# Kernel optimization log

Hardware: AMD Instinct MI355X
Metric: run time of the kernel (lower is better)

## Reference

```python
import jax, jax.numpy as jnp
import numpy as np

DIM = 1024
HEADS = 16
DIM_HEAD = 64
INNER = HEADS * DIM_HEAD  # 1024
EPS = 1e-5


def layer_norm(x, g, b):
    mu = jnp.mean(x, axis=-1, keepdims=True)
    var = jnp.var(x, axis=-1, keepdims=True)
    return (x - mu) * jax.lax.rsqrt(var + EPS) * g + b


def setup_inputs() -> dict:
    key = jax.random.key(0)
    ks = jax.random.split(key, 8)
    s = 0.02
    return {
        "x": jax.random.normal(ks[0], (2, 2048, DIM), dtype=jnp.float32),
        "w_qkv": jax.random.normal(ks[1], (DIM, 3 * INNER), dtype=jnp.float32) * s,
        "w_out": jax.random.normal(ks[2], (INNER, DIM), dtype=jnp.float32) * s,
        "b_out": jnp.zeros((DIM,), jnp.float32),
        "g1": jnp.ones((DIM,), jnp.float32),
        "bt1": jnp.zeros((DIM,), jnp.float32),
        "g2": jnp.ones((DIM,), jnp.float32),
        "bt2": jnp.zeros((DIM,), jnp.float32),
        "w1": jax.random.normal(ks[3], (DIM, DIM), dtype=jnp.float32) * s,  # ff hidden = dim_out = DIM
        "b1": jnp.zeros((DIM,), jnp.float32),
        "w2": jax.random.normal(ks[4], (DIM, DIM), dtype=jnp.float32) * s,
        "b2": jnp.zeros((DIM,), jnp.float32),
    }


def reference(x, w_qkv, w_out, b_out, g1, bt1, g2, bt2, w1, b1, w2, b2):
    b, n, _ = x.shape
    scale = DIM_HEAD ** (-0.5)
    x_in = x
    xl = layer_norm(x, g1, bt1)
    qkv = xl @ w_qkv  # [b, n, 3*inner]
    q, k, v = jnp.split(qkv, 3, axis=-1)
    def split_heads(t):
        return t.reshape(b, n, HEADS, DIM_HEAD).transpose(0, 2, 1, 3)  # b h n d
    q, k, v = map(split_heads, (q, k, v))
    dots = jnp.einsum('bhid,bhjd->bhij', q, k) * scale
    attn = jax.nn.softmax(dots, axis=-1)
    out = jnp.einsum('bhij,bhjd->bhid', attn, v)
    out = out.transpose(0, 2, 1, 3).reshape(b, n, INNER)
    out = out @ w_out + b_out
    out = out + x_in
    h = layer_norm(out, g2, bt2)
    h = jax.nn.gelu(h @ w1 + b1, approximate=False) @ w2 + b2
    return h + out
```

## Files before the change

kernel.cpp:

```cpp
#include <hip/hip_runtime.h>
#include <math.h>

typedef __attribute__((ext_vector_type(4))) float f32x4;
typedef __attribute__((ext_vector_type(8))) short bf16x8;
typedef __attribute__((ext_vector_type(8))) unsigned short u16x8;

#define DIM 1024
#define SEQ 2048
#define NHEADS 16
#define DH 64

__device__ __forceinline__ unsigned short f2bf(float f) {
    unsigned int u = __builtin_bit_cast(unsigned int, f);
    u += 0x7fffu + ((u >> 16) & 1u);
    return (unsigned short)(u >> 16);
}

__device__ __forceinline__ unsigned int cvt_pk_bf16(float lo, float hi) {
    unsigned int r;
    asm("v_cvt_pk_bf16_f32 %0, %1, %2" : "=v"(r) : "v"(lo), "v"(hi));
    return r;
}

__device__ __forceinline__ float fexp2(float x) {
    float r;
    asm("v_exp_f32 %0, %1" : "=v"(r) : "v"(x));
    return r;
}

__device__ __forceinline__ void gld16(const unsigned short* g, unsigned short* l) {
    __builtin_amdgcn_global_load_lds((const __attribute__((address_space(1))) void*)g,
                                     (__attribute__((address_space(3))) void*)l, 16, 0, 0);
}

__global__ __launch_bounds__(256) void wtrans_kernel(const float* __restrict__ w,
                                                     unsigned short* __restrict__ wt,
                                                     int K, int N, int scale_n, float sc) {
    __shared__ float t[32][33];
    int tid = threadIdx.x;
    int n0 = blockIdx.x * 32, k0 = blockIdx.y * 32;
    int c = tid & 31, rb = tid >> 5;
#pragma unroll
    for (int i = 0; i < 4; ++i) {
        int r = rb + i * 8;
        t[r][c] = w[(size_t)(k0 + r) * N + n0 + c];
    }
    __syncthreads();
#pragma unroll
    for (int i = 0; i < 4; ++i) {
        int r = rb + i * 8;
        float v = t[c][r];
        if (n0 + r < scale_n) v *= sc;
        wt[(size_t)(n0 + r) * K + k0 + c] = f2bf(v);
    }
}

__global__ __launch_bounds__(256) void ln_kernel(const float* __restrict__ x,
                                                 const float* __restrict__ g,
                                                 const float* __restrict__ bt,
                                                 unsigned short* __restrict__ o) {
    int row = blockIdx.x, tid = threadIdx.x;
    const float4* xr = (const float4*)(x + (size_t)row * DIM);
    float4 v = xr[tid];
    float s1 = v.x + v.y + v.z + v.w;
    float s2 = v.x * v.x + v.y * v.y + v.z * v.z + v.w * v.w;
#pragma unroll
    for (int m = 32; m >= 1; m >>= 1) {
        s1 += __shfl_xor(s1, m);
        s2 += __shfl_xor(s2, m);
    }
    __shared__ float r1[4], r2[4];
    int w = tid >> 6;
    if ((tid & 63) == 0) { r1[w] = s1; r2[w] = s2; }
    __syncthreads();
    s1 = r1[0] + r1[1] + r1[2] + r1[3];
    s2 = r2[0] + r2[1] + r2[2] + r2[3];
    float mu = s1 * (1.0f / DIM);
    float var = s2 * (1.0f / DIM) - mu * mu;
    float rstd = rsqrtf(var + 1e-5f);
    float4 g4 = ((const float4*)g)[tid];
    float4 b4 = ((const float4*)bt)[tid];
    ushort4 ov;
    ov.x = f2bf((v.x - mu) * rstd * g4.x + b4.x);
    ov.y = f2bf((v.y - mu) * rstd * g4.y + b4.y);
    ov.z = f2bf((v.z - mu) * rstd * g4.z + b4.z);
    ov.w = f2bf((v.w - mu) * rstd * g4.w + b4.w);
    *(ushort4*)(o + (size_t)row * DIM + tid * 4) = ov;
}

template <int BN, int OBF, int BIAS, int GELU_, int RESID>
__global__ __launch_bounds__(256) void gemm_kernel(const unsigned short* __restrict__ A,
                                                   const unsigned short* __restrict__ BT,
                                                   void* __restrict__ C,
                                                   const float* __restrict__ bias,
                                                   const float* __restrict__ resid,
                                                   int M, int N, int K, int nbx) {
    constexpr int NJ = BN / 32;
    __shared__ unsigned short As[2][128 * 32];
    __shared__ unsigned short Bs[2][BN * 32];
    int tid = threadIdx.x;
    int lane = tid & 63, w = tid >> 6;
    int l15 = lane & 15, lhi = lane >> 4;
    int nwg = gridDim.x, wg = blockIdx.x;
    int swz = (wg & 7) * (nwg >> 3) + (wg >> 3);
    int bx = swz % nbx, by = swz / nbx;
    int row0 = by * 128, col0 = bx * BN;
    int wrow = (w >> 1) * 64, wcol = (w & 1) * (16 * NJ);
    f32x4 zero = {0.f, 0.f, 0.f, 0.f};
    f32x4 acc[4][NJ];
#pragma unroll
    for (int i = 0; i < 4; ++i)
#pragma unroll
        for (int j = 0; j < NJ; ++j) acc[i][j] = zero;
    int srow = tid >> 2;
    int scol = (tid & 3) ^ ((tid >> 3) & 3);
    const unsigned short* a0 = A + (size_t)(row0 + srow) * K + scol * 8;
    const unsigned short* b0 = BT + (size_t)(col0 + srow) * K + scol * 8;
    int nk = K >> 5;
    auto stage = [&](int buf, int kt) {
        const unsigned short* ap = a0 + kt * 32;
        const unsigned short* bp = b0 + kt * 32;
        unsigned short* la = &As[buf][0] + tid * 8;
        unsigned short* lb = &Bs[buf][0] + tid * 8;
        gld16(ap, la);
        gld16(ap + (size_t)64 * K, la + 2048);
        gld16(bp, lb);
        if constexpr (BN == 128) gld16(bp + (size_t)64 * K, lb + 2048);
    };
    stage(0, 0);
    __syncthreads();
    int xr = (l15 >> 1) & 3;
    for (int kt = 0; kt < nk; ++kt) {
        int cur = kt & 1;
        if (kt + 1 < nk) stage(cur ^ 1, kt + 1);
        const unsigned short* Ab = &As[cur][0];
        const unsigned short* Bb = &Bs[cur][0];
        bf16x8 af[4], bfr[NJ];
#pragma unroll
        for (int i = 0; i < 4; ++i)
            af[i] = *(const bf16x8*)&Ab[(wrow + i * 16 + l15) * 32 + ((lhi ^ xr) * 8)];
#pragma unroll
        for (int j = 0; j < NJ; ++j)
            bfr[j] = *(const bf16x8*)&Bb[(wcol + j * 16 + l15) * 32 + ((lhi ^ xr) * 8)];
#pragma unroll
        for (int i = 0; i < 4; ++i)
#pragma unroll
            for (int j = 0; j < NJ; ++j)
                acc[i][j] = __builtin_amdgcn_mfma_f32_16x16x32_bf16(af[i], bfr[j], acc[i][j], 0, 0, 0);
        __syncthreads();
    }
#pragma unroll
    for (int i = 0; i < 4; ++i)
#pragma unroll
        for (int j = 0; j < NJ; ++j)
#pragma unroll
            for (int r = 0; r < 4; ++r) {
                int row = row0 + wrow + i * 16 + lhi * 4 + r;
                int col = col0 + wcol + j * 16 + l15;
                float v = acc[i][j][r];
                if (BIAS) v += bias[col];
                if (GELU_) v = 0.5f * v * (1.0f + erff(v * 0.70710678118f));
                if (RESID) v += resid[(size_t)row * N + col];
                if (OBF)
                    ((unsigned short*)C)[(size_t)row * N + col] = f2bf(v);
                else
                    ((float*)C)[(size_t)row * N + col] = v;
            }
}

__global__ __launch_bounds__(256) void vtrans_kernel(const unsigned short* __restrict__ qkv,
                                                     unsigned short* __restrict__ vt) {
    __shared__ unsigned short t[64 * 72];
    int tid = threadIdx.x;
    int nt = blockIdx.x & 31, h = (blockIdx.x >> 5) & 15, b = blockIdx.x >> 9;
#pragma unroll
    for (int p = 0; p < 2; ++p) {
        int c = tid + p * 256;
        int n = c >> 3, s = (c & 7) * 8;
        *(uint4*)&t[n * 72 + s] =
            *(const uint4*)(qkv + (size_t)(b * SEQ + nt * 64 + n) * 3072 + 2048 + h * 64 + s);
    }
    __syncthreads();
#pragma unroll
    for (int p = 0; p < 2; ++p) {
        int c = tid + p * 256;
        int d = c >> 3, s0 = (c & 7) * 8;
        u16x8 val;
#pragma unroll
        for (int j = 0; j < 8; ++j) {
            int s = s0 + j;
            int sig = (s & 32) | ((s & 4) << 2) | ((s & 24) >> 1) | (s & 3);
            val[j] = t[sig * 72 + d];
        }
        *(u16x8*)(vt + ((size_t)(b * NHEADS + h) * DH + d) * SEQ + nt * 64 + s0) = val;
    }
}

__global__ __launch_bounds__(256) void attn_kernel(const unsigned short* __restrict__ qkv,
                                                   const unsigned short* __restrict__ vt,
                                                   unsigned short* __restrict__ o) {
    __shared__ unsigned short Ks[2][64 * 64];
    __shared__ unsigned short Vs[2][64 * 64];
    int tid = threadIdx.x;
    int lane = tid & 63, w = tid >> 6;
    int l15 = lane & 15, lhi = lane >> 4;
    int wg = blockIdx.x;
    int swz = (wg & 7) * 64 + (wg >> 3);
    int qt = swz & 15, h = (swz >> 4) & 15, b = swz >> 8;
    bf16x8 qf[2][2];
#pragma unroll
    for (int qg = 0; qg < 2; ++qg) {
        const unsigned short* qb =
            qkv + (size_t)(b * SEQ + qt * 128 + w * 32 + qg * 16 + l15) * 3072 + h * DH;
        qf[qg][0] = *(const bf16x8*)(qb + lhi * 8);
        qf[qg][1] = *(const bf16x8*)(qb + 32 + lhi * 8);
    }
    f32x4 zero = {0.f, 0.f, 0.f, 0.f};
    f32x4 oacc[2][4], lacc[2];
#pragma unroll
    for (int qg = 0; qg < 2; ++qg) {
        lacc[qg] = zero;
#pragma unroll
        for (int i = 0; i < 4; ++i) oacc[qg][i] = zero;
    }
    const short one_s = (short)0x3F80;
    bf16x8 ones = {one_s, one_s, one_s, one_s, one_s, one_s, one_s, one_s};
    int srow = tid >> 3;
    int scx = (tid & 7) ^ (srow & 7);
    const unsigned short* kb = qkv + (size_t)b * SEQ * 3072 + 1024 + h * DH;
    const unsigned short* vb = vt + (size_t)(b * NHEADS + h) * DH * SEQ;
    const unsigned short* k0 = kb + (size_t)srow * 3072 + scx * 8;
    const unsigned short* v0 = vb + (size_t)srow * SEQ + scx * 8;
    auto stage = [&](int buf, int kt) {
        unsigned short* lk = &Ks[buf][0] + tid * 8;
        unsigned short* lv = &Vs[buf][0] + tid * 8;
        gld16(k0 + (size_t)kt * 64 * 3072, lk);
        gld16(k0 + ((size_t)kt * 64 + 32) * 3072, lk + 2048);
        gld16(v0 + kt * 64, lv);
        gld16(v0 + (size_t)32 * SEQ + kt * 64, lv + 2048);
    };
    stage(0, 0);
    __syncthreads();
    int kx = l15 & 7;
    const int NT = SEQ / 64;
    for (int kt = 0; kt < NT; ++kt) {
        int cur = kt & 1;
        if (kt + 1 < NT) stage(cur ^ 1, kt + 1);
        const unsigned short* Kc = &Ks[cur][0];
        const unsigned short* Vc = &Vs[cur][0];
        f32x4 sacc[2][4];
#pragma unroll
        for (int nt = 0; nt < 4; ++nt) {
            bf16x8 kf0 = *(const bf16x8*)&Kc[(nt * 16 + l15) * 64 + ((lhi ^ kx) * 8)];
            bf16x8 kf1 = *(const bf16x8*)&Kc[(nt * 16 + l15) * 64 + (((4 + lhi) ^ kx) * 8)];
#pragma unroll
            for (int qg = 0; qg < 2; ++qg) {
                f32x4 z = __builtin_amdgcn_mfma_f32_16x16x32_bf16(kf0, qf[qg][0], zero, 0, 0, 0);
                sacc[qg][nt] = __builtin_amdgcn_mfma_f32_16x16x32_bf16(kf1, qf[qg][1], z, 0, 0, 0);
            }
        }
        bf16x8 pf[2][2];
#pragma unroll
        for (int qg = 0; qg < 2; ++qg)
#pragma unroll
            for (int kc = 0; kc < 2; ++kc) {
                union { bf16x8 v; unsigned int u[4]; } pu;
                pu.u[0] = cvt_pk_bf16(fexp2(sacc[qg][2 * kc][0]), fexp2(sacc[qg][2 * kc][1]));
                pu.u[1] = cvt_pk_bf16(fexp2(sacc[qg][2 * kc][2]), fexp2(sacc[qg][2 * kc][3]));
                pu.u[2] = cvt_pk_bf16(fexp2(sacc[qg][2 * kc + 1][0]), fexp2(sacc[qg][2 * kc + 1][1]));
                pu.u[3] = cvt_pk_bf16(fexp2(sacc[qg][2 * kc + 1][2]), fexp2(sacc[qg][2 * kc + 1][3]));
                pf[qg][kc] = pu.v;
            }
#pragma unroll
        for (int dt = 0; dt < 4; ++dt)
#pragma unroll
            for (int kc = 0; kc < 2; ++kc) {
                bf16x8 vf = *(const bf16x8*)&Vc[(dt * 16 + l15) * 64 + (((kc * 4 + lhi) ^ kx) * 8)];
#pragma unroll
                for (int qg = 0; qg < 2; ++qg)
                    oacc[qg][dt] =
                        __builtin_amdgcn_mfma_f32_16x16x32_bf16(vf, pf[qg][kc], oacc[qg][dt], 0, 0, 0);
            }
#pragma unroll
        for (int qg = 0; qg < 2; ++qg) {
            lacc[qg] = __builtin_amdgcn_mfma_f32_16x16x32_bf16(ones, pf[qg][0], lacc[qg], 0, 0, 0);
            lacc[qg] = __builtin_amdgcn_mfma_f32_16x16x32_bf16(ones, pf[qg][1], lacc[qg], 0, 0, 0);
        }
        __syncthreads();
    }
#pragma unroll
    for (int qg = 0; qg < 2; ++qg) {
        float rl = 1.0f / lacc[qg][0];
        size_t orow = (size_t)(b * SEQ + qt * 128 + w * 32 + qg * 16 + l15) * DIM + h * DH;
#pragma unroll
        for (int dt = 0; dt < 4; ++dt) {
            ushort4 st;
            st.x = f2bf(oacc[qg][dt][0] * rl);
            st.y = f2bf(oacc[qg][dt][1] * rl);
            st.z = f2bf(oacc[qg][dt][2] * rl);
            st.w = f2bf(oacc[qg][dt][3] * rl);
            *(ushort4*)(o + orow + dt * 16 + lhi * 4) = st;
        }
    }
}

extern "C" void kernel_launch(void* const* d_in, const int* in_sizes, int n_in,
                              void* d_out, int out_size, void* d_ws, size_t ws_size,
                              hipStream_t stream) {
    (void)in_sizes; (void)n_in; (void)out_size; (void)ws_size;
    const float* x = (const float*)d_in[0];
    const float* w_qkv = (const float*)d_in[1];
    const float* w_out = (const float*)d_in[2];
    const float* b_out = (const float*)d_in[3];
    const float* g1 = (const float*)d_in[4];
    const float* bt1 = (const float*)d_in[5];
    const float* g2 = (const float*)d_in[6];
    const float* bt2 = (const float*)d_in[7];
    const float* w1 = (const float*)d_in[8];
    const float* b1 = (const float*)d_in[9];
    const float* w2 = (const float*)d_in[10];
    const float* b2 = (const float*)d_in[11];
    float* out = (float*)d_out;

    char* ws = (char*)d_ws;
    size_t off = 0;
    auto alloc = [&](size_t bytes) {
        void* p = ws + off;
        off += (bytes + 255) & ~(size_t)255;
        return p;
    };
    const int R = 2 * SEQ;
    unsigned short* xl    = (unsigned short*)alloc((size_t)R * DIM * 2);
    unsigned short* wqkvT = (unsigned short*)alloc((size_t)3 * DIM * DIM * 2);
    unsigned short* woutT = (unsigned short*)alloc((size_t)DIM * DIM * 2);
    unsigned short* w1T   = (unsigned short*)alloc((size_t)DIM * DIM * 2);
    unsigned short* w2T   = (unsigned short*)alloc((size_t)DIM * DIM * 2);
    unsigned short* qkvb  = (unsigned short*)alloc((size_t)R * 3 * DIM * 2);
    unsigned short* vtb   = (unsigned short*)alloc((size_t)R * DIM * 2);
    unsigned short* attO  = (unsigned short*)alloc((size_t)R * DIM * 2);
    unsigned short* h2    = (unsigned short*)alloc((size_t)R * DIM * 2);
    unsigned short* ffn1  = (unsigned short*)alloc((size_t)R * DIM * 2);

    const float CS = 0.125f * 1.44269504f;
    wtrans_kernel<<<dim3(3 * DIM / 32, DIM / 32), 256, 0, stream>>>(w_qkv, wqkvT, DIM, 3 * DIM, DIM, CS);
    wtrans_kernel<<<dim3(DIM / 32, DIM / 32), 256, 0, stream>>>(w_out, woutT, DIM, DIM, 0, 1.f);
    wtrans_kernel<<<dim3(DIM / 32, DIM / 32), 256, 0, stream>>>(w1, w1T, DIM, DIM, 0, 1.f);
    wtrans_kernel<<<dim3(DIM / 32, DIM / 32), 256, 0, stream>>>(w2, w2T, DIM, DIM, 0, 1.f);

    ln_kernel<<<R, 256, 0, stream>>>(x, g1, bt1, xl);
    gemm_kernel<128, 1, 0, 0, 0><<<dim3((3 * DIM / 128) * (R / 128)), 256, 0, stream>>>(
        xl, wqkvT, qkvb, nullptr, nullptr, R, 3 * DIM, DIM, 3 * DIM / 128);
    vtrans_kernel<<<2 * NHEADS * (SEQ / 64), 256, 0, stream>>>(qkvb, vtb);
    attn_kernel<<<2 * NHEADS * (SEQ / 128), 256, 0, stream>>>(qkvb, vtb, attO);
    gemm_kernel<64, 0, 1, 0, 1><<<dim3((DIM / 64) * (R / 128)), 256, 0, stream>>>(
        attO, woutT, out, b_out, x, R, DIM, DIM, DIM / 64);
    ln_kernel<<<R, 256, 0, stream>>>(out, g2, bt2, h2);
    gemm_kernel<64, 1, 1, 1, 0><<<dim3((DIM / 64) * (R / 128)), 256, 0, stream>>>(
        h2, w1T, ffn1, b1, nullptr, R, DIM, DIM, DIM / 64);
    gemm_kernel<64, 0, 1, 0, 1><<<dim3((DIM / 64) * (R / 128)), 256, 0, stream>>>(
        ffn1, w2T, out, b2, out, R, DIM, DIM, DIM / 64);
}
```

Measured before the change: 182.9 us.

## Triple-buffer GEMM and attention loads with vmcnt waits; merge weight transposes

Result: faster. 170.0 us (-7.1%).

```diff
diff --git a/kernel.cpp b/kernel.cpp
--- a/kernel.cpp
+++ b/kernel.cpp
@@ -33,12 +33,25 @@
                                      (__attribute__((address_space(3))) void*)l, 16, 0, 0);
 }
 
-__global__ __launch_bounds__(256) void wtrans_kernel(const float* __restrict__ w,
-                                                     unsigned short* __restrict__ wt,
-                                                     int K, int N, int scale_n, float sc) {
+__global__ __launch_bounds__(256) void wtrans_all(const float* __restrict__ wq,
+                                                  const float* __restrict__ wo,
+                                                  const float* __restrict__ wf1,
+                                                  const float* __restrict__ wf2,
+                                                  unsigned short* __restrict__ oq,
+                                                  unsigned short* __restrict__ oo,
+                                                  unsigned short* __restrict__ of1,
+                                                  unsigned short* __restrict__ of2, float sc) {
+    int z = blockIdx.z;
+    int bxi = blockIdx.x;
+    if (z > 0 && bxi >= 32) return;
+    const float* w = z == 0 ? wq : z == 1 ? wo : z == 2 ? wf1 : wf2;
+    unsigned short* wt = z == 0 ? oq : z == 1 ? oo : z == 2 ? of1 : of2;
+    int N = z == 0 ? 3072 : 1024;
+    int scale_n = z == 0 ? 1024 : 0;
+    const int K = 1024;
     __shared__ float t[32][33];
     int tid = threadIdx.x;
-    int n0 = blockIdx.x * 32, k0 = blockIdx.y * 32;
+    int n0 = bxi * 32, k0 = blockIdx.y * 32;
     int c = tid & 31, rb = tid >> 5;
 #pragma unroll
     for (int i = 0; i < 4; ++i) {
@@ -88,16 +101,21 @@
     *(ushort4*)(o + (size_t)row * DIM + tid * 4) = ov;
 }
 
-template <int BN, int OBF, int BIAS, int GELU_, int RESID>
+template <int BN, int BK, int OBF, int BIAS, int GELU_, int RESID>
 __global__ __launch_bounds__(256) void gemm_kernel(const unsigned short* __restrict__ A,
                                                    const unsigned short* __restrict__ BT,
                                                    void* __restrict__ C,
                                                    const float* __restrict__ bias,
                                                    const float* __restrict__ resid,
                                                    int M, int N, int K, int nbx) {
+    constexpr int U = BK / 8;
+    constexpr int NAU = 128 * U;
+    constexpr int NBU = BN * U;
+    constexpr int PT = (NAU + NBU) / 256;
     constexpr int NJ = BN / 32;
-    __shared__ unsigned short As[2][128 * 32];
-    __shared__ unsigned short Bs[2][BN * 32];
+    constexpr int KK = BK / 32;
+    __shared__ unsigned short As[3][128 * BK];
+    __shared__ unsigned short Bs[3][BN * BK];
     int tid = threadIdx.x;
     int lane = tid & 63, w = tid >> 6;
     int l15 = lane & 15, lhi = lane >> 4;
@@ -112,42 +130,69 @@
     for (int i = 0; i < 4; ++i)
 #pragma unroll
         for (int j = 0; j < NJ; ++j) acc[i][j] = zero;
-    int srow = tid >> 2;
-    int scol = (tid & 3) ^ ((tid >> 3) & 3);
-    const unsigned short* a0 = A + (size_t)(row0 + srow) * K + scol * 8;
-    const unsigned short* b0 = BT + (size_t)(col0 + srow) * K + scol * 8;
-    int nk = K >> 5;
     auto stage = [&](int buf, int kt) {
-        const unsigned short* ap = a0 + kt * 32;
-        const unsigned short* bp = b0 + kt * 32;
-        unsigned short* la = &As[buf][0] + tid * 8;
-        unsigned short* lb = &Bs[buf][0] + tid * 8;
-        gld16(ap, la);
-        gld16(ap + (size_t)64 * K, la + 2048);
-        gld16(bp, lb);
-        if constexpr (BN == 128) gld16(bp + (size_t)64 * K, lb + 2048);
+#pragma unroll
+        for (int p = 0; p < PT; ++p) {
+            if (p * 256 < NAU) {
+                int u = tid + p * 256;
+                int r = u / U, cu = u % U;
+                int scu = cu ^ (r & (U - 1));
+                gld16(A + (size_t)(row0 + r) * K + kt * BK + scu * 8, &As[buf][0] + u * 8);
+            } else {
+                int ub = tid + p * 256 - NAU;
+                int r = ub / U, cu = ub % U;
+                int scu = cu ^ (r & (U - 1));
+                gld16(BT + (size_t)(col0 + r) * K + kt * BK + scu * 8, &Bs[buf][0] + ub * 8);
+            }
+        }
     };
+    int nk = K / BK;
     stage(0, 0);
-    __syncthreads();
-    int xr = (l15 >> 1) & 3;
+    stage(1, 1);
+    asm volatile("s_waitcnt vmcnt(%0)" ::"i"(PT) : "memory");
+    __builtin_amdgcn_s_barrier();
+    __builtin_amdgcn_sched_barrier(0);
+    int cur = 0;
     for (int kt = 0; kt < nk; ++kt) {
-        int cur = kt & 1;
-        if (kt + 1 < nk) stage(cur ^ 1, kt + 1);
+        int nxt2 = cur + 2 >= 3 ? cur - 1 : cur + 2;
+        if (kt + 2 < nk) stage(nxt2, kt + 2);
         const unsigned short* Ab = &As[cur][0];
         const unsigned short* Bb = &Bs[cur][0];
-        bf16x8 af[4], bfr[NJ];
+        bf16x8 af[4][KK], bfr[NJ][KK];
 #pragma unroll
         for (int i = 0; i < 4; ++i)
-            af[i] = *(const bf16x8*)&Ab[(wrow + i * 16 + l15) * 32 + ((lhi ^ xr) * 8)];
+#pragma unroll
+            for (int kk = 0; kk < KK; ++kk) {
+                int rr = wrow + i * 16 + l15;
+                int up = (kk * 4 + lhi) ^ (rr & (U - 1));
+                af[i][kk] = *(const bf16x8*)&Ab[rr * BK + up * 8];
+            }
 #pragma unroll
         for (int j = 0; j < NJ; ++j)
-            bfr[j] = *(const bf16x8*)&Bb[(wcol + j * 16 + l15) * 32 + ((lhi ^ xr) * 8)];
-#pragma unroll
-        for (int i = 0; i < 4; ++i)
-#pragma unroll
-            for (int j = 0; j < NJ; ++j)
-                acc[i][j] = __builtin_amdgcn_mfma_f32_16x16x32_bf16(af[i], bfr[j], acc[i][j], 0, 0, 0);
-        __syncthreads();
+#pragma unroll
+            for (int kk = 0; kk < KK; ++kk) {
+                int rr = wcol + j * 16 + l15;
+                int up = (kk * 4 + lhi) ^ (rr & (U - 1));
+                bfr[j][kk] = *(const bf16x8*)&Bb[rr * BK + up * 8];
+            }
+#pragma unroll
+        for (int kk = 0; kk < KK; ++kk)
+#pragma unroll
+            for (int i = 0; i < 4; ++i)
+#pragma unroll
+                for (int j = 0; j < NJ; ++j)
+                    acc[i][j] = __builtin_amdgcn_mfma_f32_16x16x32_bf16(af[i][kk], bfr[j][kk],
+                                                                        acc[i][j], 0, 0, 0);
+        __builtin_amdgcn_sched_barrier(0);
+        if (kt + 1 < nk) {
+            if (kt + 2 < nk)
+                asm volatile("s_waitcnt vmcnt(%0)" ::"i"(PT) : "memory");
+            else
+                asm volatile("s_waitcnt vmcnt(0)" ::: "memory");
+            __builtin_amdgcn_s_barrier();
+            __builtin_amdgcn_sched_barrier(0);
+        }
+        cur = cur + 1 == 3 ? 0 : cur + 1;
     }
 #pragma unroll
     for (int i = 0; i < 4; ++i)
@@ -199,8 +244,8 @@
 __global__ __launch_bounds__(256) void attn_kernel(const unsigned short* __restrict__ qkv,
                                                    const unsigned short* __restrict__ vt,
                                                    unsigned short* __restrict__ o) {
-    __shared__ unsigned short Ks[2][64 * 64];
-    __shared__ unsigned short Vs[2][64 * 64];
+    __shared__ unsigned short Ks[3][64 * 64];
+    __shared__ unsigned short Vs[3][64 * 64];
     int tid = threadIdx.x;
     int lane = tid & 63, w = tid >> 6;
     int l15 = lane & 15, lhi = lane >> 4;
@@ -239,13 +284,17 @@
         gld16(v0 + kt * 64, lv);
         gld16(v0 + (size_t)32 * SEQ + kt * 64, lv + 2048);
     };
+    const int NT = SEQ / 64;
     stage(0, 0);
-    __syncthreads();
+    stage(1, 1);
+    asm volatile("s_waitcnt vmcnt(4)" ::: "memory");
+    __builtin_amdgcn_s_barrier();
+    __builtin_amdgcn_sched_barrier(0);
     int kx = l15 & 7;
-    const int NT = SEQ / 64;
+    int cur = 0;
     for (int kt = 0; kt < NT; ++kt) {
-        int cur = kt & 1;
-        if (kt + 1 < NT) stage(cur ^ 1, kt + 1);
+        int nxt2 = cur + 2 >= 3 ? cur - 1 : cur + 2;
+        if (kt + 2 < NT) stage(nxt2, kt + 2);
         const unsigned short* Kc = &Ks[cur][0];
         const unsigned short* Vc = &Vs[cur][0];
         f32x4 sacc[2][4];
@@ -286,7 +335,16 @@
             lacc[qg] = __builtin_amdgcn_mfma_f32_16x16x32_bf16(ones, pf[qg][0], lacc[qg], 0, 0, 0);
             lacc[qg] = __builtin_amdgcn_mfma_f32_16x16x32_bf16(ones, pf[qg][1], lacc[qg], 0, 0, 0);
         }
-        __syncthreads();
+        __builtin_amdgcn_sched_barrier(0);
+        if (kt + 1 < NT) {
+            if (kt + 2 < NT)
+                asm volatile("s_waitcnt vmcnt(4)" ::: "memory");
+            else
+                asm volatile("s_waitcnt vmcnt(0)" ::: "memory");
+            __builtin_amdgcn_s_barrier();
+            __builtin_amdgcn_sched_barrier(0);
+        }
+        cur = cur + 1 == 3 ? 0 : cur + 1;
     }
 #pragma unroll
     for (int qg = 0; qg < 2; ++qg) {
@@ -342,21 +400,18 @@
     unsigned short* ffn1  = (unsigned short*)alloc((size_t)R * DIM * 2);
 
     const float CS = 0.125f * 1.44269504f;
-    wtrans_kernel<<<dim3(3 * DIM / 32, DIM / 32), 256, 0, stream>>>(w_qkv, wqkvT, DIM, 3 * DIM, DIM, CS);
-    wtrans_kernel<<<dim3(DIM / 32, DIM / 32), 256, 0, stream>>>(w_out, woutT, DIM, DIM, 0, 1.f);
-    wtrans_kernel<<<dim3(DIM / 32, DIM / 32), 256, 0, stream>>>(w1, w1T, DIM, DIM, 0, 1.f);
-    wtrans_kernel<<<dim3(DIM / 32, DIM / 32), 256, 0, stream>>>(w2, w2T, DIM, DIM, 0, 1.f);
+    wtrans_all<<<dim3(96, 32, 4), 256, 0, stream>>>(w_qkv, w_out, w1, w2, wqkvT, woutT, w1T, w2T, CS);
 
     ln_kernel<<<R, 256, 0, stream>>>(x, g1, bt1, xl);
-    gemm_kernel<128, 1, 0, 0, 0><<<dim3((3 * DIM / 128) * (R / 128)), 256, 0, stream>>>(
+    gemm_kernel<128, 32, 1, 0, 0, 0><<<dim3((3 * DIM / 128) * (R / 128)), 256, 0, stream>>>(
         xl, wqkvT, qkvb, nullptr, nullptr, R, 3 * DIM, DIM, 3 * DIM / 128);
     vtrans_kernel<<<2 * NHEADS * (SEQ / 64), 256, 0, stream>>>(qkvb, vtb);
     attn_kernel<<<2 * NHEADS * (SEQ / 128), 256, 0, stream>>>(qkvb, vtb, attO);
-    gemm_kernel<64, 0, 1, 0, 1><<<dim3((DIM / 64) * (R / 128)), 256, 0, stream>>>(
+    gemm_kernel<64, 64, 0, 1, 0, 1><<<dim3((DIM / 64) * (R / 128)), 256, 0, stream>>>(
         attO, woutT, out, b_out, x, R, DIM, DIM, DIM / 64);
     ln_kernel<<<R, 256, 0, stream>>>(out, g2, bt2, h2);
-    gemm_kernel<64, 1, 1, 1, 0><<<dim3((DIM / 64) * (R / 128)), 256, 0, stream>>>(
+    gemm_kernel<64, 64, 1, 1, 1, 0><<<dim3((DIM / 64) * (R / 128)), 256, 0, stream>>>(
         h2, w1T, ffn1, b1, nullptr, R, DIM, DIM, DIM / 64);
-    gemm_kernel<64, 0, 1, 0, 1><<<dim3((DIM / 64) * (R / 128)), 256, 0, stream>>>(
+    gemm_kernel<64, 64, 0, 1, 0, 1><<<dim3((DIM / 64) * (R / 128)), 256, 0, stream>>>(
         ffn1, w2T, out, b2, out, R, DIM, DIM, DIM / 64);
 }
```
